# Optimization experiments

Measured on AMD Instinct MI355X. Metric: run time of the kernel, lower is better.

## Reference

```python
import jax, jax.numpy as jnp
import numpy as np
from jax import lax

B, NF, NOBJ, SZ = 16, 4, 32, 128
HALF = SZ // 2  # 64


def _build_grid(h, w):
    ys = jnp.linspace(0.0, 1.0, h)
    xs = jnp.linspace(0.0, 1.0, w)
    gy, gx = jnp.meshgrid(ys, xs, indexing='ij')
    g = jnp.stack([gy, gx], axis=-1)  # (H, W, 2)
    return jnp.concatenate([g, 1.0 - g], axis=-1)[None]  # (1, H, W, 4)


def setup_inputs() -> dict:
    key = jax.random.key(0)
    ks = jax.random.split(key, 8)
    images = jax.random.normal(ks[0], (B, 3 * NF, SZ, SZ), dtype=jnp.float32)
    rois = jax.random.randint(ks[1], (B, NOBJ, SZ, SZ), 0, 2).astype(jnp.bool_)
    conv1_w = jax.random.normal(ks[2], (64, 3 * NF, 3, 3), dtype=jnp.float32) * 0.05
    conv1_b = jnp.zeros((64,), dtype=jnp.float32)
    conv2_w = jax.random.normal(ks[3], (128, 64, 3, 3), dtype=jnp.float32) * 0.05
    conv2_b = jnp.zeros((128,), dtype=jnp.float32)
    dense_w = jax.random.normal(ks[4], (128, 4), dtype=jnp.float32) * 0.1
    dense_b = jnp.zeros((128,), dtype=jnp.float32)
    return dict(images=images, rois=rois, conv1_w=conv1_w, conv1_b=conv1_b,
                conv2_w=conv2_w, conv2_b=conv2_b, dense_w=dense_w, dense_b=dense_b)


def _conv(x, w, b):
    y = lax.conv_general_dilated(x, w, window_strides=(1, 1), padding='SAME',
                                 dimension_numbers=('NCHW', 'OIHW', 'NCHW'))
    return y + b[None, :, None, None]


def reference(images, rois, conv1_w, conv1_b, conv2_w, conv2_b, dense_w, dense_b):
    # conv stack
    x = jax.nn.relu(_conv(images, conv1_w, conv1_b))
    x = lax.reduce_window(x, -jnp.inf, lax.max, (1, 1, 2, 2), (1, 1, 2, 2), 'VALID')
    x = jax.nn.relu(_conv(x, conv2_w, conv2_b))  # (B, 128, 64, 64)
    # soft position embed
    grid = _build_grid(HALF, HALF)  # (1, 64, 64, 4)
    pe = grid @ dense_w.T + dense_b  # (1, 64, 64, 128)
    x = x + jnp.transpose(pe, (0, 3, 1, 2))  # (B, 128, 64, 64)
    # roi pool: nearest-downsample masks 128->64 (indices 0,2,4,...)
    r = rois[:, :, ::2, ::2].astype(x.dtype)  # (B, O, 64, 64)
    masked = x[:, None] * r[:, :, None]  # (B, O, 128, 64, 64)
    return jnp.max(masked, axis=(-2, -1))  # (B, O, 128)
```

## Files before the change

### kernel.cpp

```cpp
#include <hip/hip_runtime.h>


typedef __attribute__((ext_vector_type(8))) short short8;
typedef __attribute__((ext_vector_type(4))) float f32x4;
typedef __attribute__((ext_vector_type(4))) unsigned short us4;
typedef __attribute__((ext_vector_type(2))) unsigned short u16x2;
typedef unsigned short u16;
typedef unsigned int u32;

__device__ __forceinline__ u16 f2bf(float f) {
  u32 u = __builtin_bit_cast(u32, f);
  return (u16)((u + 0x7fffu + ((u >> 16) & 1u)) >> 16);
}
__device__ __forceinline__ u32 pkmaxu(u32 a, u32 b) {
  u16x2 x = __builtin_bit_cast(u16x2, a), y = __builtin_bit_cast(u16x2, b);
  return __builtin_bit_cast(u32, __builtin_elementwise_max(x, y));
}
__device__ __forceinline__ u32 map2(u32 v) {
  u32 flip = ((v & 0x80008000u) >> 15) * 0xFFFFu;
  return v ^ (flip | 0x80008000u);
}
__device__ __forceinline__ float unmap1(u32 m) {
  u32 b = m ^ ((m & 0x8000u) ? 0x8000u : 0xFFFFu);
  return __builtin_bit_cast(float, b << 16);
}

namespace {

__global__ __launch_bounds__(256) void kiop(const float* __restrict__ img,
                                            u16* __restrict__ imgT,
                                            const unsigned* __restrict__ rois,
                                            unsigned* __restrict__ rmask,
                                            const float* __restrict__ w2,
                                            u16* __restrict__ Aw2,
                                            const float* __restrict__ w1,
                                            u16* __restrict__ Aw1) {
  __shared__ alignas(16) u16 ST[2048];
  const int bx = blockIdx.x;
  const int t = threadIdx.x;
  if (bx < 2048) {
    const int row = bx & 127, b = bx >> 7;
#pragma unroll
    for (int i = 0; i < 2; ++i) {
      const int e = i * 256 + t;
      ST[(e >> 2) * 16 + 12 + (e & 3)] = 0;
    }
#pragma unroll
    for (int i = 0; i < 6; ++i) {
      const int e = i * 256 + t;
      const int ci = e >> 7, col = e & 127;
      const float v = img[(((size_t)(b * 12 + ci)) << 14) + row * 128 + col];
      ST[col * 16 + ci] = f2bf(v);
    }
    __syncthreads();
    us4* dst = (us4*)(imgT + (((size_t)(b * 128 + row)) << 11));
#pragma unroll
    for (int i = 0; i < 2; ++i) {
      const int q = i * 256 + t;
      dst[q] = *(const us4*)&ST[q * 4];
    }
  } else if (bx < 2176) {
    const int lane = t & 63;
    u32 ok = 1u;
#pragma unroll
    for (int i = 0; i < 4; ++i) {
      u32 v = rois[lane * 4 + i];
      ok &= ((v <= 1u) || (v == 0x3f800000u)) ? 1u : 0u;
    }
    const bool isWord = (__all((int)ok) != 0);
    const unsigned char* roisB = (const unsigned char*)rois;
    const int pi = (bx - 2048) * 256 + t;
    const int b = pi >> 11;
    const int pp = pi & 2047;
    const int h = pp >> 5;
    const int wp = pp & 31;
    const size_t base = (size_t)b * 32 * 16384 + (size_t)(2 * h) * 128 + 4 * wp;
    u32 m0 = 0, m1 = 0;
#pragma unroll
    for (int o = 0; o < 32; ++o) {
      const size_t idx = base + (size_t)o * 16384;
      if (isWord) {
        const uint4 q = *(const uint4*)&rois[idx];
        m0 |= (u32)(q.x != 0u) << o;
        m1 |= (u32)(q.z != 0u) << o;
      } else {
        const u32 q = *(const u32*)&roisB[idx];
        m0 |= (u32)((q & 0xffu) != 0u) << o;
        m1 |= (u32)((q & 0xff0000u) != 0u) << o;
      }
    }
    *(uint2*)&rmask[b * 4096 + h * 64 + wp * 2] = make_uint2(m0, m1);
  } else if (bx < 2464) {
    const int idx = (bx - 2176) * 256 + t;
    const int j = idx & 7;
    const int lane = (idx >> 3) & 63;
    const int t3 = idx >> 9;
    const int ks = t3 % 18, cot = t3 / 18;
    const int m = lane & 15, g = lane >> 4;
    const int co = cot * 16 + m;
    const int k = ks * 32 + g * 8 + j;
    const int rc = k >> 6, ci = k & 63;
    Aw2[idx] = f2bf(w2[co * 576 + ci * 9 + rc]);
  } else {
    const int idx = (bx - 2464) * 256 + t;
    const int j = idx & 7;
    const int lane = (idx >> 3) & 63;
    const int t3 = idx >> 9;
    const int ks = t3 % 5, cot = t3 / 5;
    const int m = lane & 15, g = lane >> 4;
    const int co = cot * 16 + m;
    const int k = ks * 32 + g * 8 + j;
    const int rc = k >> 4, cip = k & 15;
    const float v = (rc < 9 && cip < 12) ? w1[co * 108 + cip * 9 + rc] : 0.f;
    Aw1[idx] = f2bf(v);
  }
}

__global__ __launch_bounds__(256) void k1_mfma(const u16* __restrict__ imgT,
                                               const u16* __restrict__ Aw1,
                                               const float* __restrict__ b1,
                                               u16* __restrict__ pooledT) {
  __shared__ alignas(16) u16 SIMG[8192];
  __shared__ alignas(16) u16 PT[64 * 68];
  const int h2 = blockIdx.x, b = blockIdx.y;
  const int t = threadIdx.x, wv = t >> 6, l = t & 63;

#pragma unroll
  for (int i = 0; i < 4; ++i) {
    const int q = i * 256 + t;
    const int sr = q >> 8, off = q & 255;
    const int irow = 2 * h2 - 1 + sr;
    short8 v = {0, 0, 0, 0, 0, 0, 0, 0};
    if ((unsigned)irow < 128u)
      v = *(const short8*)(imgT + (((size_t)(b * 128 + irow)) << 11) + off * 8);
    *(short8*)((char*)SIMG + ((q * 16) ^ (((q >> 3) & 1) << 4))) = v;
  }
  __syncthreads();

  const int m16 = l & 15, g = l >> 4;
  const int colhalf = wv >> 1, cotbase = (wv & 1) * 2;
  const int cipb = (g & 1) * 16;
  f32x4 acc[2][8];
#pragma unroll
  for (int ct = 0; ct < 2; ++ct)
#pragma unroll
    for (int pt = 0; pt < 8; ++pt) acc[ct][pt] = (f32x4){0.f, 0.f, 0.f, 0.f};

  const u16* awb = Aw1 + (size_t)l * 8;
  const short8 z8 = {0, 0, 0, 0, 0, 0, 0, 0};

#pragma unroll
  for (int ks = 0; ks < 5; ++ks) {
    short8 a0 = *(const short8*)(awb + (cotbase * 5 + ks) * 512);
    short8 a1 = *(const short8*)(awb + ((cotbase + 1) * 5 + ks) * 512);
    const bool pz = (ks == 4) && (g >= 2);
    const int rc = pz ? 0 : (2 * ks + (g >> 1));
    const int rr = (rc * 11) >> 5;
    const int cc = rc - rr * 3;
    const int d = m16 - 1 + cc;
    const int sb = (d < 0) ? 1 : ((d >> 2) & 1);
    const int base = rr * 4096 + d * 32 + colhalf * 2048 + (cipb ^ (sb << 4));
    const bool killLo = (cc == 0) && (m16 == 0) && (colhalf == 0);
    const bool killHi = (cc == 2) && (m16 == 15) && (colhalf == 1);
#pragma unroll
    for (int pt = 0; pt < 8; ++pt) {
      const int r01 = pt >> 2, ct2 = pt & 3;
      short8 bv = *(const short8*)((const char*)SIMG + base + r01 * 4096 + ct2 * 512);
      bool kill = pz;
      if (ct2 == 0) kill = kill || killLo;
      if (ct2 == 3) kill = kill || killHi;
      if (kill) bv = z8;
      acc[0][pt] = __builtin_amdgcn_mfma_f32_16x16x32_bf16(a0, bv, acc[0][pt], 0, 0, 0);
      acc[1][pt] = __builtin_amdgcn_mfma_f32_16x16x32_bf16(a1, bv, acc[1][pt], 0, 0, 0);
    }
  }

#pragma unroll
  for (int ct = 0; ct < 2; ++ct) {
    const int cot = cotbase + ct;
#pragma unroll
    for (int r = 0; r < 4; ++r) {
      const int co = cot * 16 + g * 4 + r;
      const float bias = b1[co];
#pragma unroll
      for (int ct2 = 0; ct2 < 4; ++ct2) {
        float v0 = fmaxf(acc[ct][ct2][r] + bias, 0.f);
        float v1 = fmaxf(acc[ct][4 + ct2][r] + bias, 0.f);
        float vv = fmaxf(v0, v1);
        vv = fmaxf(vv, __shfl_xor(vv, 1, 64));
        if (!(m16 & 1)) {
          const int pw = colhalf * 32 + ct2 * 8 + (m16 >> 1);
          PT[pw * 68 + co] = f2bf(vv);
        }
      }
    }
  }
  __syncthreads();
  u16* dst = pooledT + (((size_t)(b * 64 + h2)) << 12);
#pragma unroll
  for (int i = 0; i < 4; ++i) {
    const int e = (i * 256 + t) * 4;
    const int pw = e >> 6, co = e & 63;
    *(us4*)(dst + e) = *(const us4*)&PT[pw * 68 + co];
  }
}

__global__ __launch_bounds__(256) void k2_mfma(const u16* __restrict__ pooledT,
                                               const u16* __restrict__ Aw,
                                               const float* __restrict__ b2,
                                               const float* __restrict__ dw,
                                               const float* __restrict__ db,
                                               u16* __restrict__ x2b) {
  __shared__ alignas(16) char SB[32768];
  const int hp = blockIdx.x, b = blockIdx.y;
  const int t = threadIdx.x, wv = t >> 6, l = t & 63;

#pragma unroll
  for (int i = 0; i < 8; ++i) {
    const int chunk = i * 4 + wv;
    const int row = chunk >> 3;
    const int hin = 2 * hp - 1 + row;
    short8 v = {0, 0, 0, 0, 0, 0, 0, 0};
    if ((unsigned)hin < 64u)
      v = *(const short8*)(pooledT + (((size_t)(b * 64 + hin)) << 12) +
                           ((chunk & 7) << 9) + l * 8);
    const int lin = chunk * 1024 + l * 16;
    *(short8*)(SB + (lin ^ (((lin >> 7) & 7) << 4))) = v;
  }
  __syncthreads();

  const int m16 = l & 15, g = l >> 4;
  const int kbyte = g * 16;
  f32x4 acc[2][8];
#pragma unroll
  for (int ct = 0; ct < 2; ++ct)
#pragma unroll
    for (int n = 0; n < 8; ++n) acc[ct][n] = (f32x4){0.f, 0.f, 0.f, 0.f};

  const u16* aw0 = Aw + (size_t)wv * 36 * 512 + l * 8;
  const short8 z8 = {0, 0, 0, 0, 0, 0, 0, 0};

#pragma unroll
  for (int ks = 0; ks < 18; ++ks) {
    const int rc = ks >> 1, r = rc / 3, c = rc % 3;
    const int koff = r * 8192 + (ks & 1) * 64 + kbyte;
    short8 a0 = *(const short8*)(aw0 + ks * 512);
    short8 a1 = *(const short8*)(aw0 + (18 + ks) * 512);
    const int d = m16 + c - 1;
    const int base = (koff + d * 128) ^ ((d & 7) << 4);
    const bool edgeLo = (c == 0) && (m16 == 0);
    const bool edgeHi = (c == 2) && (m16 == 15);
#pragma unroll
    for (int n = 0; n < 8; ++n) {
      const int orw = n >> 2, n4 = n & 3;
      short8 bv = *(const short8*)(SB + base + orw * 8192 + n4 * 2048);
      if (c == 0 && n4 == 0) { if (edgeLo) bv = z8; }
      if (c == 2 && n4 == 3) { if (edgeHi) bv = z8; }
      acc[0][n] = __builtin_amdgcn_mfma_f32_16x16x32_bf16(a0, bv, acc[0][n], 0, 0, 0);
      acc[1][n] = __builtin_amdgcn_mfma_f32_16x16x32_bf16(a1, bv, acc[1][n], 0, 0, 0);
    }
  }

  const float inv63 = 1.f / 63.f;
#pragma unroll
  for (int ct = 0; ct < 2; ++ct) {
    const int cot = wv * 2 + ct;
#pragma unroll
    for (int r = 0; r < 4; ++r) {
      const int co = cot * 16 + g * 4 + r;
      const float bias = b2[co];
      const float W0 = dw[co * 4 + 0], W1 = dw[co * 4 + 1];
      const float W2 = dw[co * 4 + 2], W3 = dw[co * 4 + 3];
      const float c23 = W2 + W3 + db[co];
      const float s02 = W0 - W2, s13 = W1 - W3;
#pragma unroll
      for (int orw = 0; orw < 2; ++orw) {
        const int h = 2 * hp + orw;
        const float pe0 = (float)h * inv63 * s02 + c23;
        u16* orow = x2b + (((size_t)(b * 128 + co)) << 12) + h * 64;
#pragma unroll
        for (int n4 = 0; n4 < 4; ++n4) {
          const int w = n4 * 16 + m16;
          orow[w] = f2bf(fmaxf(acc[ct][orw * 4 + n4][r] + bias, 0.f) + pe0 +
                         (float)w * inv63 * s13);
        }
      }
    }
  }
}

__global__ __launch_bounds__(256) void k3_roi(const u16* __restrict__ x2b,
                                              const unsigned* __restrict__ rmask,
                                              u32* __restrict__ partial) {
  __shared__ alignas(16) char LB[18688];
  u32* XSU = (u32*)LB;
  u32* MS = (u32*)(LB + 16640);
  const int cg = blockIdx.x, pq = blockIdx.y, b = blockIdx.z;
  const int t = threadIdx.x, wv = t >> 6, lane = t & 63;
  const int p0 = pq * 512;

#pragma unroll
  for (int i = 0; i < 4; ++i) {
    const int f4 = i * 256 + t;
    const int c = f4 >> 6, cidx = f4 & 63;
    uint4 v = *(const uint4*)&x2b[(((size_t)(b * 128 + cg * 16 + c)) << 12) + p0 + cidx * 8];
    v.x = map2(v.x); v.y = map2(v.y); v.z = map2(v.z); v.w = map2(v.w);
    *(uint4*)&XSU[c * 260 + cidx * 4] = v;
  }
  if (t < 128) *(uint4*)&MS[t * 4] = *(const uint4*)&rmask[b * 4096 + p0 + t * 4];
  __syncthreads();

  const int og = lane >> 3, cu = lane & 7;
  const u32* r0 = XSU + (2 * cu) * 260;
  const u32* r1 = XSU + (2 * cu + 1) * 260;
  const int ps = wv * 128;

  u32 a[4][2];
#pragma unroll
  for (int r = 0; r < 4; ++r) { a[r][0] = 0u; a[r][1] = 0u; }

  for (int pi = 0; pi < 32; ++pi) {
    const int p = ps + pi * 4;
    const uint4 mw = *(const uint4*)&MS[p];
    const uint2 xa = *(const uint2*)&r0[p >> 1];
    const uint2 xb = *(const uint2*)&r1[p >> 1];
#pragma unroll
    for (int r = 0; r < 4; ++r) {
      const int o = og * 4 + r;
      u32 t0 = (u32)((int)(mw.x << (31 - o)) >> 31);
      u32 t1 = (u32)((int)(mw.y << (31 - o)) >> 31);
      u32 pm = (t0 & 0xFFFFu) | (t1 & 0xFFFF0000u);
      a[r][0] = pkmaxu(a[r][0], (xa.x & pm) | (0x80008000u & ~pm));
      a[r][1] = pkmaxu(a[r][1], (xb.x & pm) | (0x80008000u & ~pm));
      t0 = (u32)((int)(mw.z << (31 - o)) >> 31);
      t1 = (u32)((int)(mw.w << (31 - o)) >> 31);
      pm = (t0 & 0xFFFFu) | (t1 & 0xFFFF0000u);
      a[r][0] = pkmaxu(a[r][0], (xa.y & pm) | (0x80008000u & ~pm));
      a[r][1] = pkmaxu(a[r][1], (xb.y & pm) | (0x80008000u & ~pm));
    }
  }

  __syncthreads();
  u32* RED = (u32*)LB;
#pragma unroll
  for (int r = 0; r < 4; ++r) {
    RED[(wv * 64 + lane) * 8 + r * 2 + 0] = a[r][0];
    RED[(wv * 64 + lane) * 8 + r * 2 + 1] = a[r][1];
  }
  __syncthreads();
  {
    const int o = t >> 3, clp = t & 7;
    const int sl = (o >> 2) * 8 + clp;
    const int s0 = (o & 3) * 2;
    u32 m0 = 0u, m1 = 0u;
#pragma unroll
    for (int w = 0; w < 4; ++w) {
      const uint2 q = *(const uint2*)&RED[(w * 64 + sl) * 8 + s0];
      m0 = pkmaxu(m0, q.x);
      m1 = pkmaxu(m1, q.y);
    }
    u32 f0l = m0 & 0xFFFFu, f0h = m0 >> 16;
    u32 f1l = m1 & 0xFFFFu, f1h = m1 >> 16;
    const u32 f0 = f0l > f0h ? f0l : f0h;
    const u32 f1 = f1l > f1h ? f1l : f1h;
    partial[(size_t)pq * 32768 + ((size_t)b * 32 + o) * 64 + cg * 8 + clp] =
        f0 | (f1 << 16);
  }
}

__global__ __launch_bounds__(256) void k4_merge(const u32* __restrict__ partial,
                                                float* __restrict__ out) {
  const int idx = blockIdx.x * 256 + threadIdx.x;
  u32 v = partial[idx];
#pragma unroll
  for (int q = 1; q < 8; ++q) v = pkmaxu(v, partial[q * 32768 + idx]);
  float2 o2;
  o2.x = unmap1(v & 0xFFFFu);
  o2.y = unmap1(v >> 16);
  *(float2*)&out[idx * 2] = o2;
}

}

extern "C" void kernel_launch(void* const* d_in, const int* in_sizes, int n_in,
                              void* d_out, int out_size, void* d_ws, size_t ws_size,
                              hipStream_t stream) {
  const float* images = (const float*)d_in[0];
  const unsigned* rois = (const unsigned*)d_in[1];
  const float* w1 = (const float*)d_in[2];
  const float* b1 = (const float*)d_in[3];
  const float* w2 = (const float*)d_in[4];
  const float* b2 = (const float*)d_in[5];
  const float* dw = (const float*)d_in[6];
  const float* db = (const float*)d_in[7];
  float* out = (float*)d_out;

  char* ws = (char*)d_ws;
  unsigned* rmask = (unsigned*)(ws);
  u16* pooledT = (u16*)(ws + 0x40000);
  u16* Aw2 = (u16*)(ws + 0x840000);
  u16* Aw1 = (u16*)(ws + 0x864000);
  u16* imgT = (u16*)(ws + 0x900000);
  u16* x2b = (u16*)(ws + 0x900000);
  u32* partial = (u32*)(ws + 0x40000);

  hipLaunchKernelGGL(kiop, dim3(2504), dim3(256), 0, stream,
                     images, imgT, rois, rmask, w2, Aw2, w1, Aw1);
  hipLaunchKernelGGL(k1_mfma, dim3(64, 16), dim3(256), 0, stream, imgT, Aw1, b1, pooledT);
  hipLaunchKernelGGL(k2_mfma, dim3(32, 16), dim3(256), 0, stream, pooledT, Aw2, b2, dw, db, x2b);
  hipLaunchKernelGGL(k3_roi, dim3(8, 8, 16), dim3(256), 0, stream, x2b, rmask, partial);
  hipLaunchKernelGGL(k4_merge, dim3(128), dim3(256), 0, stream, partial, out);
}
```

Measured before the change: 71.62 us.

## Fuse ROI max-pooling into conv2 epilogue, drop x2b intermediate

The conv2 MFMA kernel now writes its bias+ReLU+position-embedding output as mapped bf16 pairs into shared memory and immediately performs the per-object masked max over its two output rows. Each block emits a partial max slab, so the full conv2 activation tensor no longer round-trips through global memory and the separate ROI kernel launch is removed. In exchange the merge kernel now reduces 32 partial slabs instead of 8, and the fused block does serial 128-position max loops that may lengthen its tail.

```diff
diff --git a/kernel.cpp b/kernel.cpp
--- a/kernel.cpp
+++ b/kernel.cpp
@@ -205,13 +205,15 @@
   }
 }
 
-__global__ __launch_bounds__(256) void k2_mfma(const u16* __restrict__ pooledT,
-                                               const u16* __restrict__ Aw,
-                                               const float* __restrict__ b2,
-                                               const float* __restrict__ dw,
-                                               const float* __restrict__ db,
-                                               u16* __restrict__ x2b) {
+__global__ __launch_bounds__(256) void k2f(const u16* __restrict__ pooledT,
+                                           const u16* __restrict__ Aw,
+                                           const float* __restrict__ b2,
+                                           const float* __restrict__ dw,
+                                           const float* __restrict__ db,
+                                           const unsigned* __restrict__ rmask,
+                                           u32* __restrict__ partial) {
   __shared__ alignas(16) char SB[32768];
+  __shared__ u32 MS[128];
   const int hp = blockIdx.x, b = blockIdx.y;
   const int t = threadIdx.x, wv = t >> 6, l = t & 63;
 
@@ -227,6 +229,7 @@
     const int lin = chunk * 1024 + l * 16;
     *(short8*)(SB + (lin ^ (((lin >> 7) & 7) << 4))) = v;
   }
+  if (t < 128) MS[t] = rmask[b * 4096 + hp * 128 + t];
   __syncthreads();
 
   const int m16 = l & 15, g = l >> 4;
@@ -261,110 +264,64 @@
     }
   }
 
+  __syncthreads();
+
   const float inv63 = 1.f / 63.f;
 #pragma unroll
   for (int ct = 0; ct < 2; ++ct) {
     const int cot = wv * 2 + ct;
 #pragma unroll
-    for (int r = 0; r < 4; ++r) {
-      const int co = cot * 16 + g * 4 + r;
-      const float bias = b2[co];
-      const float W0 = dw[co * 4 + 0], W1 = dw[co * 4 + 1];
-      const float W2 = dw[co * 4 + 2], W3 = dw[co * 4 + 3];
-      const float c23 = W2 + W3 + db[co];
-      const float s02 = W0 - W2, s13 = W1 - W3;
+    for (int r2 = 0; r2 < 2; ++r2) {
+      const int co0 = cot * 16 + g * 4 + r2 * 2;
+      const float bias0 = b2[co0], bias1 = b2[co0 + 1];
+      const float pA0 = dw[co0 * 4 + 0] - dw[co0 * 4 + 2];
+      const float pB0 = dw[co0 * 4 + 1] - dw[co0 * 4 + 3];
+      const float pC0 = dw[co0 * 4 + 2] + dw[co0 * 4 + 3] + db[co0];
+      const float pA1 = dw[co0 * 4 + 4] - dw[co0 * 4 + 6];
+      const float pB1 = dw[co0 * 4 + 5] - dw[co0 * 4 + 7];
+      const float pC1 = dw[co0 * 4 + 6] + dw[co0 * 4 + 7] + db[co0 + 1];
 #pragma unroll
       for (int orw = 0; orw < 2; ++orw) {
-        const int h = 2 * hp + orw;
-        const float pe0 = (float)h * inv63 * s02 + c23;
-        u16* orow = x2b + (((size_t)(b * 128 + co)) << 12) + h * 64;
+        const float gy = (float)(2 * hp + orw) * inv63;
+        const float pe00 = gy * pA0 + pC0;
+        const float pe01 = gy * pA1 + pC1;
 #pragma unroll
         for (int n4 = 0; n4 < 4; ++n4) {
           const int w = n4 * 16 + m16;
-          orow[w] = f2bf(fmaxf(acc[ct][orw * 4 + n4][r] + bias, 0.f) + pe0 +
-                         (float)w * inv63 * s13);
+          const int pos = orw * 64 + w;
+          const float gx = (float)w * inv63;
+          const float v0 = fmaxf(acc[ct][orw * 4 + n4][r2 * 2 + 0] + bias0, 0.f)
+                           + pe00 + gx * pB0;
+          const float v1 = fmaxf(acc[ct][orw * 4 + n4][r2 * 2 + 1] + bias1, 0.f)
+                           + pe01 + gx * pB1;
+          const u32 pk = map2((u32)f2bf(v0) | ((u32)f2bf(v1) << 16));
+          *(u32*)(SB + ((pos * 256 + co0 * 2) ^ ((pos & 7) << 4))) = pk;
         }
       }
     }
   }
-}
-
-__global__ __launch_bounds__(256) void k3_roi(const u16* __restrict__ x2b,
-                                              const unsigned* __restrict__ rmask,
-                                              u32* __restrict__ partial) {
-  __shared__ alignas(16) char LB[18688];
-  u32* XSU = (u32*)LB;
-  u32* MS = (u32*)(LB + 16640);
-  const int cg = blockIdx.x, pq = blockIdx.y, b = blockIdx.z;
-  const int t = threadIdx.x, wv = t >> 6, lane = t & 63;
-  const int p0 = pq * 512;
-
-#pragma unroll
-  for (int i = 0; i < 4; ++i) {
-    const int f4 = i * 256 + t;
-    const int c = f4 >> 6, cidx = f4 & 63;
-    uint4 v = *(const uint4*)&x2b[(((size_t)(b * 128 + cg * 16 + c)) << 12) + p0 + cidx * 8];
-    v.x = map2(v.x); v.y = map2(v.y); v.z = map2(v.z); v.w = map2(v.w);
-    *(uint4*)&XSU[c * 260 + cidx * 4] = v;
-  }
-  if (t < 128) *(uint4*)&MS[t * 4] = *(const uint4*)&rmask[b * 4096 + p0 + t * 4];
-  __syncthreads();
-
-  const int og = lane >> 3, cu = lane & 7;
-  const u32* r0 = XSU + (2 * cu) * 260;
-  const u32* r1 = XSU + (2 * cu + 1) * 260;
-  const int ps = wv * 128;
-
-  u32 a[4][2];
-#pragma unroll
-  for (int r = 0; r < 4; ++r) { a[r][0] = 0u; a[r][1] = 0u; }
-
-  for (int pi = 0; pi < 32; ++pi) {
-    const int p = ps + pi * 4;
-    const uint4 mw = *(const uint4*)&MS[p];
-    const uint2 xa = *(const uint2*)&r0[p >> 1];
-    const uint2 xb = *(const uint2*)&r1[p >> 1];
+  __syncthreads();
+
+  const int og = t >> 5, coq = t & 31;
+  u32 a0[4], a1[4];
+#pragma unroll
+  for (int r = 0; r < 4; ++r) { a0[r] = 0u; a1[r] = 0u; }
+  for (int pos = 0; pos < 128; ++pos) {
+    const u32 mw = MS[pos];
+    const uint2 x = *(const uint2*)(SB + ((pos * 256 + coq * 8) ^ ((pos & 7) << 4)));
 #pragma unroll
     for (int r = 0; r < 4; ++r) {
       const int o = og * 4 + r;
-      u32 t0 = (u32)((int)(mw.x << (31 - o)) >> 31);
-      u32 t1 = (u32)((int)(mw.y << (31 - o)) >> 31);
-      u32 pm = (t0 & 0xFFFFu) | (t1 & 0xFFFF0000u);
-      a[r][0] = pkmaxu(a[r][0], (xa.x & pm) | (0x80008000u & ~pm));
-      a[r][1] = pkmaxu(a[r][1], (xb.x & pm) | (0x80008000u & ~pm));
-      t0 = (u32)((int)(mw.z << (31 - o)) >> 31);
-      t1 = (u32)((int)(mw.w << (31 - o)) >> 31);
-      pm = (t0 & 0xFFFFu) | (t1 & 0xFFFF0000u);
-      a[r][0] = pkmaxu(a[r][0], (xa.y & pm) | (0x80008000u & ~pm));
-      a[r][1] = pkmaxu(a[r][1], (xb.y & pm) | (0x80008000u & ~pm));
-    }
-  }
-
-  __syncthreads();
-  u32* RED = (u32*)LB;
+      const u32 am = (u32)((int)(mw << (31 - o)) >> 31);
+      a0[r] = pkmaxu(a0[r], (x.x & am) | (0x80008000u & ~am));
+      a1[r] = pkmaxu(a1[r], (x.y & am) | (0x80008000u & ~am));
+    }
+  }
+  u32* pslab = partial + (size_t)hp * 32768;
 #pragma unroll
   for (int r = 0; r < 4; ++r) {
-    RED[(wv * 64 + lane) * 8 + r * 2 + 0] = a[r][0];
-    RED[(wv * 64 + lane) * 8 + r * 2 + 1] = a[r][1];
-  }
-  __syncthreads();
-  {
-    const int o = t >> 3, clp = t & 7;
-    const int sl = (o >> 2) * 8 + clp;
-    const int s0 = (o & 3) * 2;
-    u32 m0 = 0u, m1 = 0u;
-#pragma unroll
-    for (int w = 0; w < 4; ++w) {
-      const uint2 q = *(const uint2*)&RED[(w * 64 + sl) * 8 + s0];
-      m0 = pkmaxu(m0, q.x);
-      m1 = pkmaxu(m1, q.y);
-    }
-    u32 f0l = m0 & 0xFFFFu, f0h = m0 >> 16;
-    u32 f1l = m1 & 0xFFFFu, f1h = m1 >> 16;
-    const u32 f0 = f0l > f0h ? f0l : f0h;
-    const u32 f1 = f1l > f1h ? f1l : f1h;
-    partial[(size_t)pq * 32768 + ((size_t)b * 32 + o) * 64 + cg * 8 + clp] =
-        f0 | (f1 << 16);
+    const int o = og * 4 + r;
+    *(uint2*)&pslab[((b * 32 + o) << 6) + coq * 2] = make_uint2(a0[r], a1[r]);
   }
 }
 
@@ -373,7 +330,7 @@
   const int idx = blockIdx.x * 256 + threadIdx.x;
   u32 v = partial[idx];
 #pragma unroll
-  for (int q = 1; q < 8; ++q) v = pkmaxu(v, partial[q * 32768 + idx]);
+  for (int q = 1; q < 32; ++q) v = pkmaxu(v, partial[q * 32768 + idx]);
   float2 o2;
   o2.x = unmap1(v & 0xFFFFu);
   o2.y = unmap1(v >> 16);
@@ -401,13 +358,12 @@
   u16* Aw2 = (u16*)(ws + 0x840000);
   u16* Aw1 = (u16*)(ws + 0x864000);
   u16* imgT = (u16*)(ws + 0x900000);
-  u16* x2b = (u16*)(ws + 0x900000);
-  u32* partial = (u32*)(ws + 0x40000);
+  u32* partial = (u32*)(ws + 0x900000);
 
   hipLaunchKernelGGL(kiop, dim3(2504), dim3(256), 0, stream,
                      images, imgT, rois, rmask, w2, Aw2, w1, Aw1);
   hipLaunchKernelGGL(k1_mfma, dim3(64, 16), dim3(256), 0, stream, imgT, Aw1, b1, pooledT);
-  hipLaunchKernelGGL(k2_mfma, dim3(32, 16), dim3(256), 0, stream, pooledT, Aw2, b2, dw, db, x2b);
-  hipLaunchKernelGGL(k3_roi, dim3(8, 8, 16), dim3(256), 0, stream, x2b, rmask, partial);
+  hipLaunchKernelGGL(k2f, dim3(32, 16), dim3(256), 0, stream,
+                     pooledT, Aw2, b2, dw, db, rmask, partial);
   hipLaunchKernelGGL(k4_merge, dim3(128), dim3(256), 0, stream, partial, out);
 }
```

Result: faster. 64.29 us (-10.2%).
